# Optimization experiments

Measured on AMD Instinct MI355X. Metric: run time of the kernel, lower is better.

The kernel has to match this reference:

```python
import jax, jax.numpy as jnp
import numpy as np

D = 10          # tree depth (perfect binary tree, heap layout)
K = 2           # MAX_CHILD
N = 2 ** D - 1  # nodes per tree = 1023
LD = 256        # latent_dim
B = 128         # batch of trees


def setup_inputs() -> dict:
    key = jax.random.key(0)
    ks = jax.random.split(key, 24)
    p = lambda k, shape: (jax.random.normal(k, shape, jnp.float32) * 0.05)
    return {
        "x_embed": jax.random.normal(ks[0], (B, N, LD), jnp.float32),
        "init_embedding": jax.random.normal(ks[1], (B, LD), jnp.float32),
        # leaf gates cx, ox
        "Wcx": p(ks[2], (LD, LD)), "bcx": p(ks[3], (LD,)),
        "Wox": p(ks[4], (LD, LD)), "box": p(ks[5], (LD,)),
        # token-input gates ix, fx, ux
        "Wix": p(ks[6], (LD, LD)), "bix": p(ks[7], (LD,)),
        "Wfx": p(ks[8], (LD, LD)), "bfx": p(ks[9], (LD,)),
        "Wux": p(ks[10], (LD, LD)), "bux": p(ks[11], (LD,)),
        # per-child gates: i_gates[K], f_gates[K][K], u_gates[K]
        "Wi": p(ks[12], (K, LD, LD)), "bi": p(ks[13], (K, LD)),
        "Wf": p(ks[14], (K, K, LD, LD)), "bf": p(ks[15], (K, K, LD)),
        "Wu": p(ks[16], (K, LD, LD)), "bu": p(ks[17], (K, LD)),
        # output projection oend: Linear(3*latent_dim, latent_dim)
        "Woend": p(ks[18], (3 * LD, LD)), "boend": p(ks[19], (LD,)),
    }


def _tree_lstm(x_embed, Wcx, bcx, Wox, box, Wix, bix, Wfx, bfx, Wux, bux,
               Wi, bi, Wf, bf, Wu, bu):
    lin = lambda x, W, b: x @ W + b
    # --- leaves (deepest level): c = cx(x); h = sigmoid(ox(x)) * tanh(c) ---
    leaf_start = 2 ** (D - 1) - 1
    x_leaf = x_embed[:, leaf_start:]                       # [B, 2^(D-1), d]
    c_leaf = lin(x_leaf, Wcx, bcx)
    h_leaf = jax.nn.sigmoid(lin(x_leaf, Wox, box)) * jnp.tanh(c_leaf)
    c_all = jnp.zeros_like(x_embed).at[:, leaf_start:].set(c_leaf)
    h_all = jnp.zeros_like(x_embed).at[:, leaf_start:].set(h_leaf)
    # --- internal levels, bottom-up (fixed D-1 iterations, vectorized over B*width) ---
    for lvl in range(D - 2, -1, -1):
        s, e = 2 ** lvl - 1, 2 ** (lvl + 1) - 1
        idx = np.arange(s, e)
        ch = np.stack([2 * idx + 1, 2 * idx + 2], axis=1)  # [w, K] heap children
        hch = h_all[:, ch]                                 # [B, w, K, d]
        cch = c_all[:, ch]                                 # [B, w, K, d]
        x = x_embed[:, s:e]                                # [B, w, d]
        # i = sigmoid(ix(x) + sum_k i_gates[k](h_k))
        i = jax.nn.sigmoid(lin(x, Wix, bix)
                           + jnp.einsum('bwkd,kde->bwe', hch, Wi) + bi.sum(0))
        # f_vals[k] = fx(x) + sum_j f_gates[k][j](h_j)   (NO sigmoid, faithful to source)
        f = (lin(x, Wfx, bfx)[:, :, None, :]
             + jnp.einsum('bwjd,kjde->bwke', hch, Wf) + bf.sum(1))   # [B, w, K, d]
        # u = tanh(ux(x) + sum_k u_gates[k](h_k))
        u = jnp.tanh(lin(x, Wux, bux)
                     + jnp.einsum('bwkd,kde->bwe', hch, Wu) + bu.sum(0))
        c = i * u + jnp.sum(f * cch, axis=2)
        h = jnp.tanh(c)
        c_all = c_all.at[:, s:e].set(c)
        h_all = h_all.at[:, s:e].set(h)
    return c_all[:, 0], h_all[:, 0]                        # root state (c, h)


def reference(x_embed, init_embedding, Wcx, bcx, Wox, box, Wix, bix, Wfx, bfx,
              Wux, bux, Wi, bi, Wf, bf, Wu, bu, Woend, boend):
    c_root, h_root = _tree_lstm(x_embed, Wcx, bcx, Wox, box, Wix, bix,
                                Wfx, bfx, Wux, bux, Wi, bi, Wf, bf, Wu, bu)
    s = jnp.concatenate([init_embedding, c_root, h_root], axis=1)  # [B, 3d]
    return jnp.tanh(s @ Woend + boend)                             # [B, d]
```

## Files before the change

kernel.cpp:

```cpp
#include <hip/hip_runtime.h>
#include <hip/hip_bf16.h>
#include <math.h>


#define NNODES 1023
#define BATCH  128
#define LDIM   256

typedef __attribute__((ext_vector_type(8))) short short8;
typedef __attribute__((ext_vector_type(4))) float f32x4;

__device__ __forceinline__ float sigmoidf_(float x) {
    return 1.f / (1.f + expf(-x));
}

__device__ __forceinline__ void split3(float x, ushort& h, ushort& m, ushort& l) {
    unsigned u = __float_as_uint(x);
    unsigned hu = (u + 0x7FFFu + ((u >> 16) & 1u)) & 0xFFFF0000u;
    h = (ushort)(hu >> 16);
    float r = x - __uint_as_float(hu);
    unsigned ur = __float_as_uint(r);
    unsigned mu = (ur + 0x7FFFu + ((ur >> 16) & 1u)) & 0xFFFF0000u;
    m = (ushort)(mu >> 16);
    float r2 = r - __uint_as_float(mu);
    unsigned u2 = __float_as_uint(r2);
    l = (ushort)((u2 + 0x7FFFu + ((u2 >> 16) & 1u)) >> 16);
}

struct P3 { unsigned h, m, l; };
__device__ __forceinline__ P3 pack2v(float x0, float x1) {
    ushort h0, m0, l0, h1, m1, l1;
    split3(x0, h0, m0, l0);
    split3(x1, h1, m1, l1);
    P3 r;
    r.h = (unsigned)h0 | ((unsigned)h1 << 16);
    r.m = (unsigned)m0 | ((unsigned)m1 << 16);
    r.l = (unsigned)l0 | ((unsigned)l1 << 16);
    return r;
}

__global__ __launch_bounds__(256) void build_weights(
    const float* __restrict__ Wix, const float* __restrict__ bix,
    const float* __restrict__ Wfx, const float* __restrict__ bfx,
    const float* __restrict__ Wux, const float* __restrict__ bux,
    const float* __restrict__ Wi,  const float* __restrict__ bi,
    const float* __restrict__ Wf,  const float* __restrict__ bf,
    const float* __restrict__ Wu,  const float* __restrict__ bu,
    const float* __restrict__ Wcx, const float* __restrict__ bcx,
    const float* __restrict__ Wox, const float* __restrict__ box,
    float* __restrict__ Wbig, float* __restrict__ bias_big,
    float* __restrict__ Wleaf, float* __restrict__ bias_leaf)
{
    int i = blockIdx.x * blockDim.x + threadIdx.x;
    if (i < 768 * 1024) {
        int k = i >> 10, n = i & 1023;
        int g = n >> 8, nn = n & 255;
        float v;
        if (g == 0) {
            v = (k < 256) ? Wix[k * 256 + nn]
              : (k < 512) ? Wi[(k - 256) * 256 + nn]
                          : Wi[65536 + (k - 512) * 256 + nn];
        } else if (g == 1) {
            v = (k < 256) ? Wux[k * 256 + nn]
              : (k < 512) ? Wu[(k - 256) * 256 + nn]
                          : Wu[65536 + (k - 512) * 256 + nn];
        } else {
            int kf = g - 2;
            v = (k < 256) ? Wfx[k * 256 + nn]
              : (k < 512) ? Wf[((kf * 2 + 0) * 256 + (k - 256)) * 256 + nn]
                          : Wf[((kf * 2 + 1) * 256 + (k - 512)) * 256 + nn];
        }
        Wbig[i] = v;
        return;
    }
    i -= 768 * 1024;
    if (i < 1024) {
        int g = i >> 8, nn = i & 255;
        float v;
        if (g == 0)      v = bix[nn] + bi[nn] + bi[256 + nn];
        else if (g == 1) v = bux[nn] + bu[nn] + bu[256 + nn];
        else if (g == 2) v = bfx[nn] + bf[nn] + bf[256 + nn];
        else             v = bfx[nn] + bf[512 + nn] + bf[768 + nn];
        bias_big[i] = v;
        return;
    }
    i -= 1024;
    if (i < 256 * 512) {
        int k = i >> 9, n = i & 511;
        Wleaf[i] = (n < 256) ? Wcx[k * 256 + n] : Wox[k * 256 + (n - 256)];
        return;
    }
    i -= 256 * 512;
    if (i < 512) {
        bias_leaf[i] = (i < 256) ? bcx[i] : box[i - 256];
    }
}

__global__ __launch_bounds__(256) void split_weights_T(
    const float* __restrict__ Wbig,
    ushort* __restrict__ Wth, ushort* __restrict__ Wtm, ushort* __restrict__ Wtl)
{
    __shared__ float sh[32][33];
    const int k0 = blockIdx.x * 32, n0 = blockIdx.y * 32;
    const int t = threadIdx.x;
    {
        int r = t >> 3, c4 = (t & 7) * 4;
        float4 v = *(const float4*)&Wbig[(size_t)(k0 + r) * 1024 + n0 + c4];
        sh[r][c4] = v.x; sh[r][c4 + 1] = v.y; sh[r][c4 + 2] = v.z; sh[r][c4 + 3] = v.w;
    }
    __syncthreads();
    int n = t >> 3, kc = (t & 7) * 4;
    ushort oh[4], om[4], ol[4];
#pragma unroll
    for (int j = 0; j < 4; ++j)
        split3(sh[kc + j][n], oh[j], om[j], ol[j]);
    size_t o = (size_t)(n0 + n) * 768 + k0 + kc;
    *(ushort4*)&Wth[o] = make_ushort4(oh[0], oh[1], oh[2], oh[3]);
    *(ushort4*)&Wtm[o] = make_ushort4(om[0], om[1], om[2], om[3]);
    *(ushort4*)&Wtl[o] = make_ushort4(ol[0], ol[1], ol[2], ol[3]);
}

__global__ __launch_bounds__(256, 2) void mfma_level(
    const float* __restrict__ x_embed,
    const float* __restrict__ hChild, const float* __restrict__ cChild,
    const ushort* __restrict__ Wth, const ushort* __restrict__ Wtm,
    const ushort* __restrict__ Wtl,
    const float* __restrict__ bias,
    float* __restrict__ hOut, float* __restrict__ cOut, int nstart)
{
    constexpr int AST = 40;
    __shared__ __align__(16) ushort Wlds[3][128 * AST];
    __shared__ __align__(16) ushort Vlds[3][128 * AST];

    const int tid  = threadIdx.x;
    const int node = blockIdx.x;
    const int gy   = blockIdx.y;
    const int lane = tid & 63, wid = tid >> 6;
    const int ni = wid & 1, bw = wid >> 1;
    const int srow = tid & 127, shalf = tid >> 7;

    const float* aX = x_embed + ((size_t)srow * NNODES + (nstart + node)) * LDIM;
    const float* aL = hChild + ((size_t)(2 * node) * BATCH + srow) * LDIM;
    const float* aR = aL + (size_t)BATCH * LDIM;
    const size_t nb = (size_t)(((srow >> 5) << 8) + gy * 32 + (srow & 31)) * 768;
    const ushort* w0 = Wth + nb;
    const ushort* w1 = Wtm + nb;
    const ushort* w2 = Wtl + nb;

    f32x4 acc[4][4];
#pragma unroll
    for (int g = 0; g < 4; ++g)
#pragma unroll
        for (int t2 = 0; t2 < 4; ++t2) acc[g][t2] = (f32x4){0.f, 0.f, 0.f, 0.f};

    float4 a0, a1, a2, a3;
    int4 w00, w01, w10, w11, w20, w21;

#define TREE_LOADS(IT)                                                         \
    {                                                                          \
        const int seg_  = (IT) >> 3;                                           \
        const int koff_ = ((IT) & 7) * 32 + shalf * 16;                        \
        const float* ap_ = (seg_ == 0) ? aX : (seg_ == 1) ? aL : aR;           \
        ap_ += koff_;                                                          \
        a0 = *(const float4*)(ap_);                                            \
        a1 = *(const float4*)(ap_ + 4);                                        \
        a2 = *(const float4*)(ap_ + 8);                                        \
        a3 = *(const float4*)(ap_ + 12);                                       \
        const int bko_ = (IT) * 32 + shalf * 16;                               \
        w00 = *(const int4*)(w0 + bko_); w01 = *(const int4*)(w0 + bko_ + 8);  \
        w10 = *(const int4*)(w1 + bko_); w11 = *(const int4*)(w1 + bko_ + 8);  \
        w20 = *(const int4*)(w2 + bko_); w21 = *(const int4*)(w2 + bko_ + 8);  \
    }

    TREE_LOADS(0);
    for (int it = 0; it < 24; ++it) {
        if (it) __syncthreads();
        {
            P3 p0 = pack2v(a0.x, a0.y), p1 = pack2v(a0.z, a0.w);
            P3 p2 = pack2v(a1.x, a1.y), p3 = pack2v(a1.z, a1.w);
            P3 p4 = pack2v(a2.x, a2.y), p5 = pack2v(a2.z, a2.w);
            P3 p6 = pack2v(a3.x, a3.y), p7 = pack2v(a3.z, a3.w);
            const int base = srow * AST + shalf * 16;
            *(int4*)&Vlds[0][base]     = make_int4((int)p0.h, (int)p1.h, (int)p2.h, (int)p3.h);
            *(int4*)&Vlds[0][base + 8] = make_int4((int)p4.h, (int)p5.h, (int)p6.h, (int)p7.h);
            *(int4*)&Vlds[1][base]     = make_int4((int)p0.m, (int)p1.m, (int)p2.m, (int)p3.m);
            *(int4*)&Vlds[1][base + 8] = make_int4((int)p4.m, (int)p5.m, (int)p6.m, (int)p7.m);
            *(int4*)&Vlds[2][base]     = make_int4((int)p0.l, (int)p1.l, (int)p2.l, (int)p3.l);
            *(int4*)&Vlds[2][base + 8] = make_int4((int)p4.l, (int)p5.l, (int)p6.l, (int)p7.l);
            *(int4*)&Wlds[0][base]     = w00;
            *(int4*)&Wlds[0][base + 8] = w01;
            *(int4*)&Wlds[1][base]     = w10;
            *(int4*)&Wlds[1][base + 8] = w11;
            *(int4*)&Wlds[2][base]     = w20;
            *(int4*)&Wlds[2][base + 8] = w21;
        }
        __syncthreads();
        if (it + 1 < 24) TREE_LOADS(it + 1);
        {
            short8 vf[4][3];
#pragma unroll
            for (int Nt = 0; Nt < 4; ++Nt) {
                const int rb = (bw * 64 + Nt * 16 + (lane & 15)) * AST + (lane >> 4) * 8;
#pragma unroll
                for (int s = 0; s < 3; ++s) vf[Nt][s] = *(const short8*)&Vlds[s][rb];
            }
#pragma unroll
            for (int g = 0; g < 4; ++g) {
                const int cb = (g * 32 + ni * 16 + (lane & 15)) * AST + (lane >> 4) * 8;
                short8 wh = *(const short8*)&Wlds[0][cb];
                short8 wm = *(const short8*)&Wlds[1][cb];
                short8 wl = *(const short8*)&Wlds[2][cb];
#pragma unroll
                for (int Nt = 0; Nt < 4; ++Nt)
                    acc[g][Nt] = __builtin_amdgcn_mfma_f32_16x16x32_bf16(wl, vf[Nt][0], acc[g][Nt], 0, 0, 0);
#pragma unroll
                for (int Nt = 0; Nt < 4; ++Nt)
                    acc[g][Nt] = __builtin_amdgcn_mfma_f32_16x16x32_bf16(wh, vf[Nt][2], acc[g][Nt], 0, 0, 0);
#pragma unroll
                for (int Nt = 0; Nt < 4; ++Nt)
                    acc[g][Nt] = __builtin_amdgcn_mfma_f32_16x16x32_bf16(wm, vf[Nt][1], acc[g][Nt], 0, 0, 0);
#pragma unroll
                for (int Nt = 0; Nt < 4; ++Nt)
                    acc[g][Nt] = __builtin_amdgcn_mfma_f32_16x16x32_bf16(wm, vf[Nt][0], acc[g][Nt], 0, 0, 0);
#pragma unroll
                for (int Nt = 0; Nt < 4; ++Nt)
                    acc[g][Nt] = __builtin_amdgcn_mfma_f32_16x16x32_bf16(wh, vf[Nt][1], acc[g][Nt], 0, 0, 0);
#pragma unroll
                for (int Nt = 0; Nt < 4; ++Nt)
                    acc[g][Nt] = __builtin_amdgcn_mfma_f32_16x16x32_bf16(wh, vf[Nt][0], acc[g][Nt], 0, 0, 0);
            }
        }
    }
#undef TREE_LOADS

    const int nc = gy * 32 + ni * 16 + ((lane >> 4) << 2);
    const size_t cLb = (size_t)(2 * node) * BATCH * LDIM;
    const size_t cRb = cLb + (size_t)BATCH * LDIM;
    const size_t ob  = (size_t)node * BATCH * LDIM;
    const float4 bi4 = *(const float4*)&bias[nc];
    const float4 bu4 = *(const float4*)&bias[256 + nc];
    const float4 b04 = *(const float4*)&bias[512 + nc];
    const float4 b14 = *(const float4*)&bias[768 + nc];
    const float bi_[4] = {bi4.x, bi4.y, bi4.z, bi4.w};
    const float bu_[4] = {bu4.x, bu4.y, bu4.z, bu4.w};
    const float b0_[4] = {b04.x, b04.y, b04.z, b04.w};
    const float b1_[4] = {b14.x, b14.y, b14.z, b14.w};
#pragma unroll
    for (int Nt = 0; Nt < 4; ++Nt) {
        const int b = bw * 64 + Nt * 16 + (lane & 15);
        float4 cL = *(const float4*)&cChild[cLb + (size_t)b * LDIM + nc];
        float4 cR = *(const float4*)&cChild[cRb + (size_t)b * LDIM + nc];
        float cl4[4] = {cL.x, cL.y, cL.z, cL.w};
        float cr4[4] = {cR.x, cR.y, cR.z, cR.w};
        float4 c4, h4;
        float* cp = (float*)&c4; float* hp = (float*)&h4;
#pragma unroll
        for (int j = 0; j < 4; ++j) {
            float gi = sigmoidf_(acc[0][Nt][j] + bi_[j]);
            float gu = tanhf(acc[1][Nt][j] + bu_[j]);
            float f0 = acc[2][Nt][j] + b0_[j];
            float f1 = acc[3][Nt][j] + b1_[j];
            float c  = gi * gu + f0 * cl4[j] + f1 * cr4[j];
            cp[j] = c;
            hp[j] = tanhf(c);
        }
        *(float4*)&cOut[ob + (size_t)b * LDIM + nc] = c4;
        *(float4*)&hOut[ob + (size_t)b * LDIM + nc] = h4;
    }
}

__global__ __launch_bounds__(256) void leaf_kernel(
    const float* __restrict__ x_embed,
    const float* __restrict__ Wleaf, const float* __restrict__ bias_leaf,
    float* __restrict__ hOut, float* __restrict__ cOut)
{
    __shared__ float As[16 * 68];
    __shared__ float Bs[2 * 16 * 64];
    float acc[2][4][4] = {};
    const int tid = threadIdx.x;
    const int ty = tid >> 4, tx = tid & 15;
    const int row0 = blockIdx.x * 64;
    const int n0 = blockIdx.y * 64;
    const int w = row0 >> 7;
    const int ar = tid >> 2;
    const int kq = (tid & 3) * 4;
    const int b = (row0 + ar) & 127;
    const float* xrow = x_embed + ((size_t)b * NNODES + 511 + w) * LDIM;

    for (int k0 = 0; k0 < 256; k0 += 16) {
        float4 av = *(const float4*)(xrow + k0 + kq);
        As[(kq + 0) * 68 + ar] = av.x;
        As[(kq + 1) * 68 + ar] = av.y;
        As[(kq + 2) * 68 + ar] = av.z;
        As[(kq + 3) * 68 + ar] = av.w;
#pragma unroll
        for (int q = 0; q < 2; ++q) {
            int L = q * 256 + tid;
            int g = L >> 8, kk = (L >> 4) & 15, n4 = (L & 15) * 4;
            float4 bv = *(const float4*)(Wleaf + (size_t)(k0 + kk) * 512 + g * 256 + n0 + n4);
            *(float4*)&Bs[(g * 16 + kk) * 64 + n4] = bv;
        }
        __syncthreads();
#pragma unroll
        for (int kk = 0; kk < 16; ++kk) {
            float4 a = *(const float4*)&As[kk * 68 + ty * 4];
            float av4[4] = {a.x, a.y, a.z, a.w};
#pragma unroll
            for (int g = 0; g < 2; ++g) {
                float4 bb = *(const float4*)&Bs[(g * 16 + kk) * 64 + tx * 4];
                float bv4[4] = {bb.x, bb.y, bb.z, bb.w};
#pragma unroll
                for (int ii = 0; ii < 4; ++ii)
#pragma unroll
                    for (int jj = 0; jj < 4; ++jj)
                        acc[g][ii][jj] += av4[ii] * bv4[jj];
            }
        }
        __syncthreads();
    }
#pragma unroll
    for (int ii = 0; ii < 4; ++ii) {
        int r = row0 + ty * 4 + ii;
        int nc = n0 + tx * 4;
        float4 c4, h4;
        float* cp = (float*)&c4; float* hp = (float*)&h4;
#pragma unroll
        for (int jj = 0; jj < 4; ++jj) {
            int n = nc + jj;
            float ac = acc[0][ii][jj] + bias_leaf[n];
            float ao = acc[1][ii][jj] + bias_leaf[256 + n];
            cp[jj] = ac;
            hp[jj] = sigmoidf_(ao) * tanhf(ac);
        }
        *(float4*)&cOut[(size_t)r * LDIM + nc] = c4;
        *(float4*)&hOut[(size_t)r * LDIM + nc] = h4;
    }
}

__global__ __launch_bounds__(256) void level_kernel(
    const float* __restrict__ x_embed,
    const float* __restrict__ hChild, const float* __restrict__ cChild,
    const float* __restrict__ Wbig, const float* __restrict__ bias_big,
    float* __restrict__ hOut, float* __restrict__ cOut,
    int nstart)
{
    __shared__ float As[16 * 68];
    __shared__ float Bs[4 * 16 * 64];
    float acc[4][4][4] = {};
    const int tid = threadIdx.x;
    const int ty = tid >> 4, tx = tid & 15;
    const int row0 = blockIdx.x * 64;
    const int n0 = blockIdx.y * 64;
    const int w = row0 >> 7;
    const int ar = tid >> 2;
    const int kq = (tid & 3) * 4;
    const int b = (row0 + ar) & 127;
    const float* srcX = x_embed + ((size_t)b * NNODES + nstart + w) * LDIM;
    const float* srcL = hChild + ((size_t)(2 * w) * BATCH + b) * LDIM;
    const float* srcR = hChild + ((size_t)(2 * w + 1) * BATCH + b) * LDIM;

    for (int k0 = 0; k0 < 768; k0 += 16) {
        int seg = k0 >> 8, off = k0 & 255;
        const float* src = (seg == 0) ? srcX : (seg == 1) ? srcL : srcR;
        float4 av = *(const float4*)(src + off + kq);
        As[(kq + 0) * 68 + ar] = av.x;
        As[(kq + 1) * 68 + ar] = av.y;
        As[(kq + 2) * 68 + ar] = av.z;
        As[(kq + 3) * 68 + ar] = av.w;
#pragma unroll
        for (int q = 0; q < 4; ++q) {
            int L = q * 256 + tid;
            int g = L >> 8, kk = (L >> 4) & 15, n4 = (L & 15) * 4;
            float4 bv = *(const float4*)(Wbig + (size_t)(k0 + kk) * 1024 + g * 256 + n0 + n4);
            *(float4*)&Bs[(g * 16 + kk) * 64 + n4] = bv;
        }
        __syncthreads();
#pragma unroll
        for (int kk = 0; kk < 16; ++kk) {
            float4 a = *(const float4*)&As[kk * 68 + ty * 4];
            float av4[4] = {a.x, a.y, a.z, a.w};
#pragma unroll
            for (int g = 0; g < 4; ++g) {
                float4 bb = *(const float4*)&Bs[(g * 16 + kk) * 64 + tx * 4];
                float bv4[4] = {bb.x, bb.y, bb.z, bb.w};
#pragma unroll
                for (int ii = 0; ii < 4; ++ii)
#pragma unroll
                    for (int jj = 0; jj < 4; ++jj)
                        acc[g][ii][jj] += av4[ii] * bv4[jj];
            }
        }
        __syncthreads();
    }
    const size_t cLbase = ((size_t)(2 * w) * BATCH) * LDIM;
    const size_t cRbase = ((size_t)(2 * w + 1) * BATCH) * LDIM;
#pragma unroll
    for (int ii = 0; ii < 4; ++ii) {
        int r = row0 + ty * 4 + ii;
        int bb2 = r & 127;
        int nc = n0 + tx * 4;
        float4 cL = *(const float4*)&cChild[cLbase + (size_t)bb2 * LDIM + nc];
        float4 cR = *(const float4*)&cChild[cRbase + (size_t)bb2 * LDIM + nc];
        float cl4[4] = {cL.x, cL.y, cL.z, cL.w};
        float cr4[4] = {cR.x, cR.y, cR.z, cR.w};
        float4 c4, h4;
        float* cp = (float*)&c4; float* hp = (float*)&h4;
#pragma unroll
        for (int jj = 0; jj < 4; ++jj) {
            int n = nc + jj;
            float gi = sigmoidf_(acc[0][ii][jj] + bias_big[n]);
            float gu = tanhf(acc[1][ii][jj] + bias_big[256 + n]);
            float f0 = acc[2][ii][jj] + bias_big[512 + n];
            float f1 = acc[3][ii][jj] + bias_big[768 + n];
            float c = gi * gu + f0 * cl4[jj] + f1 * cr4[jj];
            cp[jj] = c;
            hp[jj] = tanhf(c);
        }
        *(float4*)&cOut[(size_t)r * LDIM + nc] = c4;
        *(float4*)&hOut[(size_t)r * LDIM + nc] = h4;
    }
}

__global__ __launch_bounds__(256) void gemm_part4(
    const float* __restrict__ x_embed, const float* __restrict__ hChild,
    const float* __restrict__ Wbig,
    float* __restrict__ part, int nstart, int rowsTotal)
{
    __shared__ float As[16 * 68];
    __shared__ float Bs[4 * 16 * 64];
    float acc[4][4][4] = {};
    const int tid = threadIdx.x;
    const int ty = tid >> 4, tx = tid & 15;
    const int row0 = blockIdx.x * 64;
    const int n0 = blockIdx.y * 64;
    const int seg = blockIdx.z;
    const int w = row0 >> 7;
    const int ar = tid >> 2;
    const int kq = (tid & 3) * 4;
    const int b = (row0 + ar) & 127;
    const float* src =
        (seg == 0) ? x_embed + ((size_t)b * NNODES + nstart + w) * LDIM
                   : hChild + ((size_t)(2 * w + (seg - 1)) * BATCH + b) * LDIM;

    for (int k0 = 0; k0 < 256; k0 += 16) {
        float4 av = *(const float4*)(src + k0 + kq);
        As[(kq + 0) * 68 + ar] = av.x;
        As[(kq + 1) * 68 + ar] = av.y;
        As[(kq + 2) * 68 + ar] = av.z;
        As[(kq + 3) * 68 + ar] = av.w;
#pragma unroll
        for (int q = 0; q < 4; ++q) {
            int L = q * 256 + tid;
            int g = L >> 8, kk = (L >> 4) & 15, n4 = (L & 15) * 4;
            float4 bv = *(const float4*)(Wbig + (size_t)(seg * 256 + k0 + kk) * 1024
                                         + g * 256 + n0 + n4);
            *(float4*)&Bs[(g * 16 + kk) * 64 + n4] = bv;
        }
        __syncthreads();
#pragma unroll
        for (int kk = 0; kk < 16; ++kk) {
            float4 a = *(const float4*)&As[kk * 68 + ty * 4];
            float av4[4] = {a.x, a.y, a.z, a.w};
#pragma unroll
            for (int g = 0; g < 4; ++g) {
                float4 bb = *(const float4*)&Bs[(g * 16 + kk) * 64 + tx * 4];
                float bv4[4] = {bb.x, bb.y, bb.z, bb.w};
#pragma unroll
                for (int ii = 0; ii < 4; ++ii)
#pragma unroll
                    for (int jj = 0; jj < 4; ++jj)
                        acc[g][ii][jj] += av4[ii] * bv4[jj];
            }
        }
        __syncthreads();
    }
#pragma unroll
    for (int ii = 0; ii < 4; ++ii) {
        int r = row0 + ty * 4 + ii;
        size_t base = ((size_t)seg * rowsTotal + r) * 1024 + n0 + tx * 4;
#pragma unroll
        for (int g = 0; g < 4; ++g)
            *(float4*)&part[base + g * 256] = *(float4*)acc[g][ii];
    }
}

__global__ __launch_bounds__(256) void combine_eps(
    const float* __restrict__ part, const float* __restrict__ cChild,
    const float* __restrict__ bias,
    float* __restrict__ hOut, float* __restrict__ cOut, int rowsTotal)
{
    int idx = blockIdx.x * 256 + threadIdx.x;
    int row = idx >> 6, n = (idx & 63) * 4;
    size_t sseg = (size_t)rowsTotal * 1024;
    const float* p0 = part + (size_t)row * 1024 + n;
    float s[4][4];
#pragma unroll
    for (int g = 0; g < 4; ++g) {
        float4 a = *(const float4*)(p0 + g * 256);
        float4 b = *(const float4*)(p0 + sseg + g * 256);
        float4 c = *(const float4*)(p0 + 2 * sseg + g * 256);
        s[g][0] = a.x + b.x + c.x; s[g][1] = a.y + b.y + c.y;
        s[g][2] = a.z + b.z + c.z; s[g][3] = a.w + b.w + c.w;
    }
    int node = row >> 7, b = row & 127;
    float4 cL = *(const float4*)&cChild[((size_t)(2 * node) * BATCH + b) * LDIM + n];
    float4 cR = *(const float4*)&cChild[((size_t)(2 * node + 1) * BATCH + b) * LDIM + n];
    float cl4[4] = {cL.x, cL.y, cL.z, cL.w};
    float cr4[4] = {cR.x, cR.y, cR.z, cR.w};
    float4 c4, h4;
    float* cp = (float*)&c4; float* hp = (float*)&h4;
#pragma unroll
    for (int jj = 0; jj < 4; ++jj) {
        int nn = n + jj;
        float gi = sigmoidf_(s[0][jj] + bias[nn]);
        float gu = tanhf(s[1][jj] + bias[256 + nn]);
        float f0 = s[2][jj] + bias[512 + nn];
        float f1 = s[3][jj] + bias[768 + nn];
        float c = gi * gu + f0 * cl4[jj] + f1 * cr4[jj];
        cp[jj] = c;
        hp[jj] = tanhf(c);
    }
    *(float4*)&cOut[(size_t)row * LDIM + n] = c4;
    *(float4*)&hOut[(size_t)row * LDIM + n] = h4;
}

__global__ __launch_bounds__(256) void final_kernel(
    const float* __restrict__ init_emb,
    const float* __restrict__ cRoot, const float* __restrict__ hRoot,
    const float* __restrict__ Woend, const float* __restrict__ boend,
    float* __restrict__ out)
{
    __shared__ float sv[768];
    int b = blockIdx.x, t = threadIdx.x;
    sv[t]       = init_emb[(size_t)b * 256 + t];
    sv[256 + t] = cRoot[(size_t)b * 256 + t];
    sv[512 + t] = hRoot[(size_t)b * 256 + t];
    __syncthreads();
    float acc = boend[t];
#pragma unroll 4
    for (int d = 0; d < 768; ++d)
        acc += sv[d] * Woend[(size_t)d * 256 + t];
    out[(size_t)b * 256 + t] = tanhf(acc);
}

extern "C" void kernel_launch(void* const* d_in, const int* in_sizes, int n_in,
                              void* d_out, int out_size, void* d_ws, size_t ws_size,
                              hipStream_t stream)
{
    const float* x_embed  = (const float*)d_in[0];
    const float* init_emb = (const float*)d_in[1];
    const float* Wcx = (const float*)d_in[2];  const float* bcx = (const float*)d_in[3];
    const float* Wox = (const float*)d_in[4];  const float* box = (const float*)d_in[5];
    const float* Wix = (const float*)d_in[6];  const float* bix = (const float*)d_in[7];
    const float* Wfx = (const float*)d_in[8];  const float* bfx = (const float*)d_in[9];
    const float* Wux = (const float*)d_in[10]; const float* bux = (const float*)d_in[11];
    const float* Wi  = (const float*)d_in[12]; const float* bi  = (const float*)d_in[13];
    const float* Wf  = (const float*)d_in[14]; const float* bf  = (const float*)d_in[15];
    const float* Wu  = (const float*)d_in[16]; const float* bu  = (const float*)d_in[17];
    const float* Woend = (const float*)d_in[18]; const float* boend = (const float*)d_in[19];
    float* out = (float*)d_out;
    float* ws  = (float*)d_ws;

    size_t off = 0;
    float* hA = ws + off; off += (size_t)512 * 128 * 256;
    float* cA = ws + off; off += (size_t)512 * 128 * 256;
    float* hB = ws + off; off += (size_t)256 * 128 * 256;
    float* cB = ws + off; off += (size_t)256 * 128 * 256;
    float* Wbig      = ws + off; off += (size_t)768 * 1024;
    float* bias_big  = ws + off; off += 1024;
    float* Wleaf     = ws + off; off += (size_t)256 * 512;
    float* bias_leaf = ws + off; off += 512;
    ushort* Wth = (ushort*)(ws + off); off += (size_t)768 * 1024 / 2;
    ushort* Wtm = (ushort*)(ws + off); off += (size_t)768 * 1024 / 2;
    ushort* Wtl = (ushort*)(ws + off); off += (size_t)768 * 1024 / 2;
    size_t mfma_need = off * sizeof(float);
    size_t part_off = off;
    float* part = ws + part_off;

    bool mfma_ok = mfma_need <= ws_size;

    {
        int total = 768 * 1024 + 1024 + 256 * 512 + 512;
        int blocks = (total + 255) / 256;
        build_weights<<<blocks, 256, 0, stream>>>(
            Wix, bix, Wfx, bfx, Wux, bux, Wi, bi, Wf, bf, Wu, bu,
            Wcx, bcx, Wox, box, Wbig, bias_big, Wleaf, bias_leaf);
    }
    if (mfma_ok) {
        split_weights_T<<<dim3(24, 32), 256, 0, stream>>>(Wbig, Wth, Wtm, Wtl);
    }

    leaf_kernel<<<dim3(1024, 4), 256, 0, stream>>>(x_embed, Wleaf, bias_leaf, hA, cA);

    float* hbufs[2] = {hA, hB};
    float* cbufs[2] = {cA, cB};
    int child = 0;
    for (int lvl = 8; lvl >= 0; --lvl) {
        int W = 1 << lvl, s = W - 1;
        int outb = child ^ 1;
        size_t rows = (size_t)W * 128;
        bool split = (W <= 16) &&
                     ((part_off + 3 * rows * 1024) * sizeof(float) <= ws_size);
        if (lvl >= 5 && mfma_ok) {
            mfma_level<<<dim3(W, 8), 256, 0, stream>>>(
                x_embed, hbufs[child], cbufs[child], Wth, Wtm, Wtl, bias_big,
                hbufs[outb], cbufs[outb], s);
        } else if (split) {
            gemm_part4<<<dim3(W * 2, 4, 3), 256, 0, stream>>>(
                x_embed, hbufs[child], Wbig, part, s, (int)rows);
            combine_eps<<<(int)(rows / 4), 256, 0, stream>>>(
                part, cbufs[child], bias_big, hbufs[outb], cbufs[outb], (int)rows);
        } else {
            level_kernel<<<dim3(W * 2, 4), 256, 0, stream>>>(
                x_embed, hbufs[child], cbufs[child], Wbig, bias_big,
                hbufs[outb], cbufs[outb], s);
        }
        child = outb;
    }

    final_kernel<<<128, 256, 0, stream>>>(init_emb, cbufs[child], hbufs[child],
                                          Woend, boend, out);
}
```

Measured before the change: 1.272 ms.

## Pre-split inputs and child hidden states into bf16 planes for MFMA levels

Adds a split_x kernel that converts x_embed for internal nodes into three bf16 planes (hi/mid/lo) in node-major layout. The leaf and MFMA level kernels now also write the hidden state as bf16 planes. The new mfma_level_ps loads these pre-split operands directly, so it no longer splits fp32 values inside the K loop. This removes repeated conversion ALU work and halves per-plane load width. The cost is an extra pass over x_embed, extra plane writes per level, and a larger workspace, and this path is used only when the workspace is big enough.

```diff
diff --git a/kernel.cpp b/kernel.cpp
--- a/kernel.cpp
+++ b/kernel.cpp
@@ -120,7 +120,185 @@
     *(ushort4*)&Wtl[o] = make_ushort4(ol[0], ol[1], ol[2], ol[3]);
 }
 
-__global__ __launch_bounds__(256, 2) void mfma_level(
+__global__ __launch_bounds__(256) void split_x(
+    const float* __restrict__ x_embed,
+    ushort* __restrict__ xs0, ushort* __restrict__ xs1, ushort* __restrict__ xs2)
+{
+    int q = blockIdx.x * 256 + threadIdx.x;
+    if (q >= 511 * 128 * 64) return;
+    int d4 = (q & 63) * 4;
+    int b = (q >> 6) & 127;
+    int node = q >> 13;
+    float4 v = *(const float4*)&x_embed[((size_t)b * NNODES + node) * LDIM + d4];
+    float vv[4] = {v.x, v.y, v.z, v.w};
+    ushort sh[4], sm[4], sl[4];
+#pragma unroll
+    for (int j = 0; j < 4; ++j) split3(vv[j], sh[j], sm[j], sl[j]);
+    size_t o = ((size_t)node * BATCH + b) * LDIM + d4;
+    *(ushort4*)&xs0[o] = make_ushort4(sh[0], sh[1], sh[2], sh[3]);
+    *(ushort4*)&xs1[o] = make_ushort4(sm[0], sm[1], sm[2], sm[3]);
+    *(ushort4*)&xs2[o] = make_ushort4(sl[0], sl[1], sl[2], sl[3]);
+}
+
+__global__ __launch_bounds__(256, 2) void mfma_level_ps(
+    const ushort* __restrict__ xs0, const ushort* __restrict__ xs1,
+    const ushort* __restrict__ xs2,
+    const ushort* __restrict__ hi0, const ushort* __restrict__ hi1,
+    const ushort* __restrict__ hi2,
+    const float* __restrict__ cChild,
+    const ushort* __restrict__ Wth, const ushort* __restrict__ Wtm,
+    const ushort* __restrict__ Wtl,
+    const float* __restrict__ bias,
+    float* __restrict__ hOut,
+    ushort* __restrict__ ho0, ushort* __restrict__ ho1, ushort* __restrict__ ho2,
+    float* __restrict__ cOut, int nstart)
+{
+    constexpr int AST = 40;
+    __shared__ __align__(16) ushort Wlds[3][128 * AST];
+    __shared__ __align__(16) ushort Vlds[3][128 * AST];
+
+    const int tid  = threadIdx.x;
+    const int node = blockIdx.x;
+    const int gy   = blockIdx.y;
+    const int lane = tid & 63, wid = tid >> 6;
+    const int ni = wid & 1, bw = wid >> 1;
+    const int srow = tid & 127, shalf = tid >> 7;
+
+    const size_t xoff = ((size_t)(nstart + node) * BATCH + srow) * LDIM;
+    const size_t loff = ((size_t)(2 * node) * BATCH + srow) * LDIM;
+    const size_t roff = loff + (size_t)BATCH * LDIM;
+    const size_t nb = (size_t)(((srow >> 5) << 8) + gy * 32 + (srow & 31)) * 768;
+    const ushort* w0 = Wth + nb;
+    const ushort* w1 = Wtm + nb;
+    const ushort* w2 = Wtl + nb;
+
+    f32x4 acc[4][4];
+#pragma unroll
+    for (int g = 0; g < 4; ++g)
+#pragma unroll
+        for (int t2 = 0; t2 < 4; ++t2) acc[g][t2] = (f32x4){0.f, 0.f, 0.f, 0.f};
+
+    int4 v00, v01, v10, v11, v20, v21;
+    int4 w00, w01, w10, w11, w20, w21;
+
+#define TREE_LOADS(IT)                                                         \
+    {                                                                          \
+        const int seg_  = (IT) >> 3;                                           \
+        const size_t o_ = (seg_ == 0 ? xoff : (seg_ == 1 ? loff : roff))       \
+                          + ((IT) & 7) * 32 + shalf * 16;                      \
+        const ushort* p0_ = (seg_ == 0) ? xs0 : hi0;                           \
+        const ushort* p1_ = (seg_ == 0) ? xs1 : hi1;                           \
+        const ushort* p2_ = (seg_ == 0) ? xs2 : hi2;                           \
+        v00 = *(const int4*)(p0_ + o_); v01 = *(const int4*)(p0_ + o_ + 8);    \
+        v10 = *(const int4*)(p1_ + o_); v11 = *(const int4*)(p1_ + o_ + 8);    \
+        v20 = *(const int4*)(p2_ + o_); v21 = *(const int4*)(p2_ + o_ + 8);    \
+        const int bko_ = (IT) * 32 + shalf * 16;                               \
+        w00 = *(const int4*)(w0 + bko_); w01 = *(const int4*)(w0 + bko_ + 8);  \
+        w10 = *(const int4*)(w1 + bko_); w11 = *(const int4*)(w1 + bko_ + 8);  \
+        w20 = *(const int4*)(w2 + bko_); w21 = *(const int4*)(w2 + bko_ + 8);  \
+    }
+
+    TREE_LOADS(0);
+    for (int it = 0; it < 24; ++it) {
+        if (it) __syncthreads();
+        {
+            const int base = srow * AST + shalf * 16;
+            *(int4*)&Vlds[0][base]     = v00;
+            *(int4*)&Vlds[0][base + 8] = v01;
+            *(int4*)&Vlds[1][base]     = v10;
+            *(int4*)&Vlds[1][base + 8] = v11;
+            *(int4*)&Vlds[2][base]     = v20;
+            *(int4*)&Vlds[2][base + 8] = v21;
+            *(int4*)&Wlds[0][base]     = w00;
+            *(int4*)&Wlds[0][base + 8] = w01;
+            *(int4*)&Wlds[1][base]     = w10;
+            *(int4*)&Wlds[1][base + 8] = w11;
+            *(int4*)&Wlds[2][base]     = w20;
+            *(int4*)&Wlds[2][base + 8] = w21;
+        }
+        __syncthreads();
+        if (it + 1 < 24) TREE_LOADS(it + 1);
+        {
+            short8 vf[4][3];
+#pragma unroll
+            for (int Nt = 0; Nt < 4; ++Nt) {
+                const int rb = (bw * 64 + Nt * 16 + (lane & 15)) * AST + (lane >> 4) * 8;
+#pragma unroll
+                for (int s = 0; s < 3; ++s) vf[Nt][s] = *(const short8*)&Vlds[s][rb];
+            }
+#pragma unroll
+            for (int g = 0; g < 4; ++g) {
+                const int cb = (g * 32 + ni * 16 + (lane & 15)) * AST + (lane >> 4) * 8;
+                short8 wh = *(const short8*)&Wlds[0][cb];
+                short8 wm = *(const short8*)&Wlds[1][cb];
+                short8 wl = *(const short8*)&Wlds[2][cb];
+#pragma unroll
+                for (int Nt = 0; Nt < 4; ++Nt)
+                    acc[g][Nt] = __builtin_amdgcn_mfma_f32_16x16x32_bf16(wl, vf[Nt][0], acc[g][Nt], 0, 0, 0);
+#pragma unroll
+                for (int Nt = 0; Nt < 4; ++Nt)
+                    acc[g][Nt] = __builtin_amdgcn_mfma_f32_16x16x32_bf16(wh, vf[Nt][2], acc[g][Nt], 0, 0, 0);
+#pragma unroll
+                for (int Nt = 0; Nt < 4; ++Nt)
+                    acc[g][Nt] = __builtin_amdgcn_mfma_f32_16x16x32_bf16(wm, vf[Nt][1], acc[g][Nt], 0, 0, 0);
+#pragma unroll
+                for (int Nt = 0; Nt < 4; ++Nt)
+                    acc[g][Nt] = __builtin_amdgcn_mfma_f32_16x16x32_bf16(wm, vf[Nt][0], acc[g][Nt], 0, 0, 0);
+#pragma unroll
+                for (int Nt = 0; Nt < 4; ++Nt)
+                    acc[g][Nt] = __builtin_amdgcn_mfma_f32_16x16x32_bf16(wh, vf[Nt][1], acc[g][Nt], 0, 0, 0);
+#pragma unroll
+                for (int Nt = 0; Nt < 4; ++Nt)
+                    acc[g][Nt] = __builtin_amdgcn_mfma_f32_16x16x32_bf16(wh, vf[Nt][0], acc[g][Nt], 0, 0, 0);
+            }
+        }
+    }
+#undef TREE_LOADS
+
+    const int nc = gy * 32 + ni * 16 + ((lane >> 4) << 2);
+    const size_t cLb = (size_t)(2 * node) * BATCH * LDIM;
+    const size_t cRb = cLb + (size_t)BATCH * LDIM;
+    const size_t ob  = (size_t)node * BATCH * LDIM;
+    const float4 bi4 = *(const float4*)&bias[nc];
+    const float4 bu4 = *(const float4*)&bias[256 + nc];
+    const float4 b04 = *(const float4*)&bias[512 + nc];
+    const float4 b14 = *(const float4*)&bias[768 + nc];
+    const float bi_[4] = {bi4.x, bi4.y, bi4.z, bi4.w};
+    const float bu_[4] = {bu4.x, bu4.y, bu4.z, bu4.w};
+    const float b0_[4] = {b04.x, b04.y, b04.z, b04.w};
+    const float b1_[4] = {b14.x, b14.y, b14.z, b14.w};
+#pragma unroll
+    for (int Nt = 0; Nt < 4; ++Nt) {
+        const int b = bw * 64 + Nt * 16 + (lane & 15);
+        float4 cL = *(const float4*)&cChild[cLb + (size_t)b * LDIM + nc];
+        float4 cR = *(const float4*)&cChild[cRb + (size_t)b * LDIM + nc];
+        float cl4[4] = {cL.x, cL.y, cL.z, cL.w};
+        float cr4[4] = {cR.x, cR.y, cR.z, cR.w};
+        float4 c4, h4;
+        float* cp = (float*)&c4; float* hp = (float*)&h4;
+        ushort sh[4], sm[4], sl[4];
+#pragma unroll
+        for (int j = 0; j < 4; ++j) {
+            float gi = sigmoidf_(acc[0][Nt][j] + bi_[j]);
+            float gu = tanhf(acc[1][Nt][j] + bu_[j]);
+            float f0 = acc[2][Nt][j] + b0_[j];
+            float f1 = acc[3][Nt][j] + b1_[j];
+            float c  = gi * gu + f0 * cl4[j] + f1 * cr4[j];
+            float h  = tanhf(c);
+            cp[j] = c;
+            hp[j] = h;
+            split3(h, sh[j], sm[j], sl[j]);
+        }
+        size_t po = ob + (size_t)b * LDIM + nc;
+        *(float4*)&cOut[po] = c4;
+        *(float4*)&hOut[po] = h4;
+        *(ushort4*)&ho0[po] = make_ushort4(sh[0], sh[1], sh[2], sh[3]);
+        *(ushort4*)&ho1[po] = make_ushort4(sm[0], sm[1], sm[2], sm[3]);
+        *(ushort4*)&ho2[po] = make_ushort4(sl[0], sl[1], sl[2], sl[3]);
+    }
+}
+
+__global__ __launch_bounds__(256, 2) void mfma_level_pack(
     const float* __restrict__ x_embed,
     const float* __restrict__ hChild, const float* __restrict__ cChild,
     const ushort* __restrict__ Wth, const ushort* __restrict__ Wtm,
@@ -272,7 +450,9 @@
 __global__ __launch_bounds__(256) void leaf_kernel(
     const float* __restrict__ x_embed,
     const float* __restrict__ Wleaf, const float* __restrict__ bias_leaf,
-    float* __restrict__ hOut, float* __restrict__ cOut)
+    float* __restrict__ hOut, float* __restrict__ cOut,
+    ushort* __restrict__ hp0, ushort* __restrict__ hp1, ushort* __restrict__ hp2,
+    int writePlanes)
 {
     __shared__ float As[16 * 68];
     __shared__ float Bs[2 * 16 * 64];
@@ -324,16 +504,25 @@
         int nc = n0 + tx * 4;
         float4 c4, h4;
         float* cp = (float*)&c4; float* hp = (float*)&h4;
+        ushort sh[4], sm[4], sl[4];
 #pragma unroll
         for (int jj = 0; jj < 4; ++jj) {
             int n = nc + jj;
             float ac = acc[0][ii][jj] + bias_leaf[n];
             float ao = acc[1][ii][jj] + bias_leaf[256 + n];
+            float h = sigmoidf_(ao) * tanhf(ac);
             cp[jj] = ac;
-            hp[jj] = sigmoidf_(ao) * tanhf(ac);
-        }
-        *(float4*)&cOut[(size_t)r * LDIM + nc] = c4;
-        *(float4*)&hOut[(size_t)r * LDIM + nc] = h4;
+            hp[jj] = h;
+            split3(h, sh[jj], sm[jj], sl[jj]);
+        }
+        size_t po = (size_t)r * LDIM + nc;
+        *(float4*)&cOut[po] = c4;
+        *(float4*)&hOut[po] = h4;
+        if (writePlanes) {
+            *(ushort4*)&hp0[po] = make_ushort4(sh[0], sh[1], sh[2], sh[3]);
+            *(ushort4*)&hp1[po] = make_ushort4(sm[0], sm[1], sm[2], sm[3]);
+            *(ushort4*)&hp2[po] = make_ushort4(sl[0], sl[1], sl[2], sl[3]);
+        }
     }
 }
 
@@ -574,9 +763,18 @@
     ushort* Wtm = (ushort*)(ws + off); off += (size_t)768 * 1024 / 2;
     ushort* Wtl = (ushort*)(ws + off); off += (size_t)768 * 1024 / 2;
     size_t mfma_need = off * sizeof(float);
+    const size_t hpa_sz = (size_t)512 * 128 * 256 / 2;
+    const size_t hpb_sz = (size_t)256 * 128 * 256 / 2;
+    const size_t xs_sz  = (size_t)511 * 128 * 256 / 2;
+    ushort* hpA[3]; ushort* hpB[3]; ushort* xs[3];
+    for (int s = 0; s < 3; ++s) { hpA[s] = (ushort*)(ws + off); off += hpa_sz; }
+    for (int s = 0; s < 3; ++s) { hpB[s] = (ushort*)(ws + off); off += hpb_sz; }
+    for (int s = 0; s < 3; ++s) { xs[s]  = (ushort*)(ws + off); off += xs_sz; }
+    size_t presplit_need = off * sizeof(float);
     size_t part_off = off;
     float* part = ws + part_off;
 
+    bool presplit_ok = presplit_need <= ws_size;
     bool mfma_ok = mfma_need <= ws_size;
 
     {
@@ -589,11 +787,20 @@
     if (mfma_ok) {
         split_weights_T<<<dim3(24, 32), 256, 0, stream>>>(Wbig, Wth, Wtm, Wtl);
     }
-
-    leaf_kernel<<<dim3(1024, 4), 256, 0, stream>>>(x_embed, Wleaf, bias_leaf, hA, cA);
+    if (presplit_ok) {
+        split_x<<<(511 * 128 * 64 + 255) / 256, 256, 0, stream>>>(
+            x_embed, xs[0], xs[1], xs[2]);
+    }
+
+    leaf_kernel<<<dim3(1024, 4), 256, 0, stream>>>(
+        x_embed, Wleaf, bias_leaf, hA, cA,
+        hpA[0], hpA[1], hpA[2], presplit_ok ? 1 : 0);
 
     float* hbufs[2] = {hA, hB};
     float* cbufs[2] = {cA, cB};
+    ushort* hp0bufs[2] = {hpA[0], hpB[0]};
+    ushort* hp1bufs[2] = {hpA[1], hpB[1]};
+    ushort* hp2bufs[2] = {hpA[2], hpB[2]};
     int child = 0;
     for (int lvl = 8; lvl >= 0; --lvl) {
         int W = 1 << lvl, s = W - 1;
@@ -601,8 +808,15 @@
         size_t rows = (size_t)W * 128;
         bool split = (W <= 16) &&
                      ((part_off + 3 * rows * 1024) * sizeof(float) <= ws_size);
-        if (lvl >= 5 && mfma_ok) {
-            mfma_level<<<dim3(W, 8), 256, 0, stream>>>(
+        if (lvl >= 5 && presplit_ok) {
+            mfma_level_ps<<<dim3(W, 8), 256, 0, stream>>>(
+                xs[0], xs[1], xs[2],
+                hp0bufs[child], hp1bufs[child], hp2bufs[child],
+                cbufs[child], Wth, Wtm, Wtl, bias_big,
+                hbufs[outb], hp0bufs[outb], hp1bufs[outb], hp2bufs[outb],
+                cbufs[outb], s);
+        } else if (lvl >= 5 && mfma_ok) {
+            mfma_level_pack<<<dim3(W, 8), 256, 0, stream>>>(
                 x_embed, hbufs[child], cbufs[child], Wth, Wtm, Wtl, bias_big,
                 hbufs[outb], cbufs[outb], s);
         } else if (split) {
```

Result: slower. 1.496 ms (+17.6%).
